# Performance work log

Measured on AMD Instinct MI355X. Metric: run time of the kernel, lower is better.

## Reference

```python
import jax, jax.numpy as jnp
import numpy as np

B, S, FEAT, HID, H = 8, 1024, 1024, 1024, 8
DH = HID // H  # head dim = 128
MASK_VAL = -128.0  # mask_val = -2**7 (soft additive mask, per original code)


def setup_inputs() -> dict:
    key = jax.random.key(0)
    ks = jax.random.split(key, 4)
    scale = 0.02
    return {
        "queries": jax.random.normal(ks[0], (B, S, FEAT), dtype=jnp.float32),
        "Wq": jax.random.normal(ks[1], (FEAT, HID), dtype=jnp.float32) * scale,
        "bq": jnp.zeros((HID,), dtype=jnp.float32),
        "Wk": jax.random.normal(ks[2], (FEAT, HID), dtype=jnp.float32) * scale,
        "bk": jnp.zeros((HID,), dtype=jnp.float32),
        "Wv": jax.random.normal(ks[3], (FEAT, HID), dtype=jnp.float32) * scale,
        "bv": jnp.zeros((HID,), dtype=jnp.float32),
    }


def reference(queries, Wq, bq, Wk, bk, Wv, bv):
    # Self-attention: keys = values = queries (torch forward defaults)
    q = queries @ Wq + bq  # [B,S,HID]
    k = queries @ Wk + bk
    v = queries @ Wv + bv
    # split heads: chunk along last dim == reshape (B,S,H,DH)
    qh = q.reshape(B, S, H, DH)
    kh = k.reshape(B, S, H, DH)
    vh = v.reshape(B, S, H, DH)
    # exp-scaled-dot score (non-standard: exp BEFORE mask/softmax)
    logits = jnp.einsum("bqhd,bkhd->bhqk", qh, kh) / np.float32(np.sqrt(DH))
    score = jnp.exp(logits)
    # soft additive causal mask: upper triangle (diag=1) gets -128
    mask = jnp.triu(jnp.full((S, S), MASK_VAL, dtype=score.dtype), k=1)
    att = jax.nn.softmax(score + mask, axis=-1)  # [B,H,S,S]
    ctx = jnp.einsum("bhqk,bkhd->bqhd", att, vh)  # [B,S,H,DH]
    # reverse heads: concat along last dim
    return ctx.reshape(B, S, HID)
```

## Files before the change

kernel.cpp:

```cpp
#include <hip/hip_runtime.h>


typedef __bf16 bf16x8 __attribute__((ext_vector_type(8)));
typedef float floatx4 __attribute__((ext_vector_type(4)));
typedef unsigned short u16;
typedef unsigned int u32;

#define RSCALE 0.08838834764831845f

__device__ __forceinline__ u16 f2b(float f) {
  union { float f; unsigned u; } v; v.f = f;
  return (u16)((v.u + 0x7FFFu + ((v.u >> 16) & 1u)) >> 16);
}

__device__ __forceinline__ void gld_lds16(const void* g, void* l) {
  __builtin_amdgcn_global_load_lds(
      (const __attribute__((address_space(1))) unsigned*)g,
      (__attribute__((address_space(3))) unsigned*)l, 16, 0, 0);
}

#define MFMA16(a, b, c) __builtin_amdgcn_mfma_f32_16x16x32_bf16(a, b, c, 0, 0, 0)

__global__ __launch_bounds__(256) void prep_kernel(
    const float4* __restrict__ X, u16* __restrict__ Xb,
    const float* __restrict__ Wq, const float* __restrict__ Wk,
    const float* __restrict__ Wv, u16* __restrict__ Wtb) {
  if (blockIdx.x < 8192) {
    unsigned i = blockIdx.x * 256u + threadIdx.x;
    float4 v = X[i];
    ushort4 o;
    o.x = f2b(v.x); o.y = f2b(v.y); o.z = f2b(v.z); o.w = f2b(v.w);
    *reinterpret_cast<ushort4*>(Xb + 4u * i) = o;
  } else {
    const int bid = blockIdx.x - 8192;
    const int mat = bid >> 10;
    const int bx = bid & 31, by = (bid >> 5) & 31;
    const float* W = (mat == 0) ? Wq : (mat == 1) ? Wk : Wv;
    u16* Wt = Wtb + (size_t)mat * (1024u * 1024u);
    __shared__ u16 tile[32][33];
    const int x = threadIdx.x & 31, y = threadIdx.x >> 5;
    const int kt = bx * 32, nt = by * 32;
#pragma unroll
    for (int i = 0; i < 4; ++i)
      tile[y + 8 * i][x] = f2b(W[(size_t)(kt + y + 8 * i) * 1024 + nt + x]);
    __syncthreads();
#pragma unroll
    for (int i = 0; i < 4; ++i)
      Wt[(size_t)(nt + y + 8 * i) * 1024 + kt + x] = tile[x][y + 8 * i];
  }
}

__global__ __launch_bounds__(256, 2) void gemm_qkv_kernel(
    const u16* __restrict__ Xb, const u16* __restrict__ Wtb,
    const float* __restrict__ bq, const float* __restrict__ bk,
    const float* __restrict__ bv, u16* __restrict__ Qh, u16* __restrict__ Kh,
    u16* __restrict__ Vt) {
  const int mat = blockIdx.z;
  const u16* __restrict__ Wt = Wtb + (size_t)mat * (1024u * 1024u);
  const float* __restrict__ bias = (mat == 0) ? bq : (mat == 1) ? bk : bv;

  const int m0 = blockIdx.x * 128;
  const int n0 = blockIdx.y * 128;

  __shared__ u16 As[2][128 * 64];
  __shared__ u16 Bs[2][128 * 64];

  const int tid = threadIdx.x;
  const int wid = tid >> 6;
  const int lane = tid & 63;
  const int quad = lane >> 4;
  const int l16 = lane & 15;
  const int wm = (wid & 1) * 64;
  const int wn = (wid >> 1) * 64;

  const floatx4 z4 = {0.f, 0.f, 0.f, 0.f};
  floatx4 acc[4][4];
#pragma unroll
  for (int i = 0; i < 4; ++i)
#pragma unroll
    for (int j = 0; j < 4; ++j) acc[i][j] = z4;

  const int srow = wid * 32;
  const int lrow = lane >> 3;
  const int gblk = (lane & 7) ^ lrow;

  auto stage = [&](int b, int k0) {
#pragma unroll
    for (int c = 0; c < 4; ++c) {
      const int row = srow + c * 8 + lrow;
      gld_lds16(Xb + (size_t)(m0 + row) * 1024 + k0 + gblk * 8,
                As[b] + (srow + c * 8) * 64);
      gld_lds16(Wt + (size_t)(n0 + row) * 1024 + k0 + gblk * 8,
                Bs[b] + (srow + c * 8) * 64);
    }
  };

  stage(0, 0);

  for (int i = 0; i < 16; ++i) {
    __syncthreads();
    if (i < 15) stage((i + 1) & 1, (i + 1) * 64);

    const u16* __restrict__ Ab = As[i & 1];
    const u16* __restrict__ Bb = Bs[i & 1];
#pragma unroll
    for (int c = 0; c < 2; ++c) {
      const int phys = ((c * 4 + quad) ^ (l16 & 7)) * 8;
      bf16x8 af[4], bfr[4];
#pragma unroll
      for (int ii = 0; ii < 4; ++ii)
        af[ii] = *(const bf16x8*)(Ab + (wm + ii * 16 + l16) * 64 + phys);
#pragma unroll
      for (int j = 0; j < 4; ++j)
        bfr[j] = *(const bf16x8*)(Bb + (wn + j * 16 + l16) * 64 + phys);
#pragma unroll
      for (int ii = 0; ii < 4; ++ii)
#pragma unroll
        for (int j = 0; j < 4; ++j)
          acc[ii][j] = MFMA16(af[ii], bfr[j], acc[ii][j]);
    }
  }

  const int b = m0 >> 10;
  const int h = n0 >> 7;
  const int sbase = (m0 & 1023) + wm;
  float bv4[4];
#pragma unroll
  for (int j = 0; j < 4; ++j) bv4[j] = bias[n0 + wn + j * 16 + l16];

  if (mat < 2) {
    u16* outp = (mat == 0 ? Qh : Kh) + (size_t)(b * 8 + h) * 1024 * 128;
#pragma unroll
    for (int i = 0; i < 4; ++i)
#pragma unroll
      for (int j = 0; j < 4; ++j) {
        const int d = wn + j * 16 + l16;
#pragma unroll
        for (int r = 0; r < 4; ++r) {
          const int s = sbase + i * 16 + quad * 4 + r;
          outp[(size_t)s * 128 + d] = f2b(acc[i][j][r] + bv4[j]);
        }
      }
  } else {
    u16* outp = Vt + (size_t)(b * 8 + h) * 128 * 1024;
#pragma unroll
    for (int i = 0; i < 4; ++i)
#pragma unroll
      for (int j = 0; j < 4; ++j) {
        const int d = wn + j * 16 + l16;
        const int s = sbase + i * 16 + quad * 4;
        ushort4 pk;
        pk.x = f2b(acc[i][j][0] + bv4[j]);
        pk.y = f2b(acc[i][j][1] + bv4[j]);
        pk.z = f2b(acc[i][j][2] + bv4[j]);
        pk.w = f2b(acc[i][j][3] + bv4[j]);
        *(ushort4*)(outp + (size_t)d * 1024 + s) = pk;
      }
  }
}

__global__ __launch_bounds__(256, 2) void attn_kernel(const u16* __restrict__ Qh,
                                                      const u16* __restrict__ Kh,
                                                      const u16* __restrict__ Vt,
                                                      float* __restrict__ out) {
  const int id = blockIdx.x;
  const int x = id & 7;
  const int j = id >> 3;
  const int bh = x * 8 + (j & 7);
  const int QTMAP[8] = {7, 5, 6, 4, 0, 2, 1, 3};
  const int qt = QTMAP[j >> 3];
  const int q0 = qt * 128;

  const int tid = threadIdx.x;
  const int wid = tid >> 6;
  const int lane = tid & 63;
  const int quad = lane >> 4;
  const int l16 = lane & 15;

  __shared__ u16 Ks[2][64 * 128];
  __shared__ u16 Vs[2][128 * 64];
  __shared__ u16 Ps[4][32 * 32];

  const u16* __restrict__ Qbase = Qh + (size_t)bh * 1024 * 128;
  const u16* __restrict__ Kbase = Kh + (size_t)bh * 1024 * 128;
  const u16* __restrict__ Vbase = Vt + (size_t)bh * 128 * 1024;

  const int qw = q0 + wid * 32;

  bf16x8 qf[2][4];
#pragma unroll
  for (int nt = 0; nt < 2; ++nt)
#pragma unroll
    for (int c = 0; c < 4; ++c)
      qf[nt][c] = *(const bf16x8*)(Qbase + (size_t)(qw + nt * 16 + l16) * 128 +
                                   c * 32 + quad * 8);

  const floatx4 z4 = {0.f, 0.f, 0.f, 0.f};
  floatx4 o[2][8];
#pragma unroll
  for (int nt = 0; nt < 2; ++nt)
#pragma unroll
    for (int dt = 0; dt < 8; ++dt) o[nt][dt] = z4;
  float lacc[2] = {0.f, 0.f};

  auto stage = [&](int b, int k0) {
#pragma unroll
    for (int c = 0; c < 4; ++c) {
      const int r0 = wid * 16 + c * 4;
      const int row = r0 + quad;
      gld_lds16(Kbase + (size_t)(k0 + row) * 128 + ((l16 ^ (c * 4 + quad)) * 8),
                Ks[b] + r0 * 128);
    }
#pragma unroll
    for (int c = 0; c < 4; ++c) {
      const int r0 = wid * 32 + c * 8;
      const int row = r0 + (lane >> 3);
      gld_lds16(Vbase + (size_t)row * 1024 + k0 +
                    (((lane & 7) ^ ((lane >> 3) & 7)) * 8),
                Vs[b] + r0 * 64);
    }
  };

  const int n = (q0 + 128) >> 6;
  stage(0, 0);

  for (int i = 0; i < n; ++i) {
    const int k0 = i << 6;
    __syncthreads();
    if (i + 1 < n) stage((i + 1) & 1, k0 + 64);

    const u16* __restrict__ Kb = Ks[i & 1];
    const u16* __restrict__ Vb = Vs[i & 1];

#pragma unroll
    for (int half = 0; half < 2; ++half) {
      if (k0 + half * 32 > qw + 31) break;

#pragma unroll
      for (int f2 = 0; f2 < 2; ++f2) {
        const int f = half * 2 + f2;
        bf16x8 kf[4];
#pragma unroll
        for (int c = 0; c < 4; ++c)
          kf[c] = *(const bf16x8*)(Kb + (f * 16 + l16) * 128 +
                                   (((c * 4 + quad) ^ l16) * 8));
        floatx4 st[2];
#pragma unroll
        for (int nt = 0; nt < 2; ++nt) {
          st[nt] = z4;
#pragma unroll
          for (int c = 0; c < 4; ++c) st[nt] = MFMA16(kf[c], qf[nt][c], st[nt]);
        }
        const int kb = k0 + f * 16 + quad * 4;
#pragma unroll
        for (int nt = 0; nt < 2; ++nt) {
          const int qrow = qw + nt * 16 + l16;
          float p[4];
#pragma unroll
          for (int r = 0; r < 4; ++r) {
            const float e = fminf(__expf(st[nt][r] * RSCALE), 85.f);
            p[r] = (kb + r > qrow) ? 0.f : __expf(e);
          }
          lacc[nt] += (p[0] + p[1]) + (p[2] + p[3]);
          uint2 pk;
          pk.x = (u32)f2b(p[0]) | ((u32)f2b(p[1]) << 16);
          pk.y = (u32)f2b(p[2]) | ((u32)f2b(p[3]) << 16);
          *(uint2*)((char*)Ps[wid] + (nt * 16 + l16) * 64 +
                    (((f2 * 2 + (quad >> 1)) ^ (l16 & 3)) * 16) +
                    (quad & 1) * 8) = pk;
        }
      }
      asm volatile("s_waitcnt lgkmcnt(0)" ::: "memory");

      bf16x8 pa[2];
#pragma unroll
      for (int nt = 0; nt < 2; ++nt)
        pa[nt] = *(const bf16x8*)((char*)Ps[wid] + (nt * 16 + l16) * 64 +
                                  ((quad ^ (l16 & 3)) * 16));
#pragma unroll
      for (int dt = 0; dt < 8; ++dt) {
        const bf16x8 vf = *(const bf16x8*)(
            Vb + (dt * 16 + l16) * 64 +
            (((half * 4 + quad) ^ (l16 & 7)) * 8));
        o[0][dt] = MFMA16(vf, pa[0], o[0][dt]);
        o[1][dt] = MFMA16(vf, pa[1], o[1][dt]);
      }
    }
  }

  float linv[2];
#pragma unroll
  for (int nt = 0; nt < 2; ++nt) {
    float s = lacc[nt];
    s += __shfl_xor(s, 16);
    s += __shfl_xor(s, 32);
    linv[nt] = 1.0f / s;
  }

  float* outp = out + (size_t)(bh >> 3) * 1024 * 1024 + (bh & 7) * 128;
#pragma unroll
  for (int nt = 0; nt < 2; ++nt) {
    const int qrow = qw + nt * 16 + l16;
#pragma unroll
    for (int dt = 0; dt < 8; ++dt) {
      float4 v;
      v.x = o[nt][dt][0] * linv[nt];
      v.y = o[nt][dt][1] * linv[nt];
      v.z = o[nt][dt][2] * linv[nt];
      v.w = o[nt][dt][3] * linv[nt];
      *(float4*)(outp + (size_t)qrow * 1024 + dt * 16 + quad * 4) = v;
    }
  }
}

extern "C" void kernel_launch(void* const* d_in, const int* in_sizes, int n_in,
                              void* d_out, int out_size, void* d_ws,
                              size_t ws_size, hipStream_t stream) {
  const float* X = (const float*)d_in[0];
  const float* Wq = (const float*)d_in[1];
  const float* bq = (const float*)d_in[2];
  const float* Wk = (const float*)d_in[3];
  const float* bk = (const float*)d_in[4];
  const float* Wv = (const float*)d_in[5];
  const float* bv = (const float*)d_in[6];
  float* out = (float*)d_out;

  char* ws = (char*)d_ws;
  u16* Xb  = (u16*)(ws);
  u16* Wtb = (u16*)(ws + (16u << 20));
  u16* Qh  = (u16*)(ws + (22u << 20));
  u16* Kh  = (u16*)(ws + (38u << 20));
  u16* Vt  = (u16*)(ws + (54u << 20));

  prep_kernel<<<8192 + 3072, 256, 0, stream>>>((const float4*)X, Xb, Wq, Wk,
                                               Wv, Wtb);
  dim3 gg(64, 8, 3);
  gemm_qkv_kernel<<<gg, 256, 0, stream>>>(Xb, Wtb, bq, bk, bv, Qh, Kh, Vt);
  attn_kernel<<<512, 256, 0, stream>>>(Qh, Kh, Vt, out);
}
```

Measured before the change: 198.7 us.

## Keep P in registers via permuted V layout, fold scale into Wq, shrink KV tiles

The attention kernel no longer round-trips the probability tile through shared memory. It packs P directly into MFMA operand registers and reads V in a key order that matches the accumulator layout, which removes the LDS write, the wait and the reload. The KV tile shrinks from 64 to 32 keys, and the causal mask is applied only on the diagonal tile. The softmax scale and log2e are folded into Wq and the bias so that exp2 can be used directly. The bf16 conversion switches from round-to-nearest-even to cheaper round-half-up with perm packing, which changes numerics slightly, and the smaller tiles add more iterations and barriers.

```diff
diff --git a/kernel.cpp b/kernel.cpp
--- a/kernel.cpp
+++ b/kernel.cpp
@@ -3,14 +3,22 @@
 
 typedef __bf16 bf16x8 __attribute__((ext_vector_type(8)));
 typedef float floatx4 __attribute__((ext_vector_type(4)));
+typedef unsigned int u32x4 __attribute__((ext_vector_type(4)));
+typedef unsigned long long u64;
+typedef u64 u64x2 __attribute__((ext_vector_type(2)));
 typedef unsigned short u16;
 typedef unsigned int u32;
 
-#define RSCALE 0.08838834764831845f
-
-__device__ __forceinline__ u16 f2b(float f) {
-  union { float f; unsigned u; } v; v.f = f;
-  return (u16)((v.u + 0x7FFFu + ((v.u >> 16) & 1u)) >> 16);
+#define LOG2E 1.4426950408889634f
+#define QSCALE 0.12751743f
+#define PSEL 0x07060302u
+
+__device__ __forceinline__ u32 pkbf16(float lo, float hi) {
+  return __builtin_amdgcn_perm(__float_as_uint(hi) + 0x8000u,
+                               __float_as_uint(lo) + 0x8000u, PSEL);
+}
+__device__ __forceinline__ u16 b16(float f) {
+  return (u16)((__float_as_uint(f) + 0x8000u) >> 16);
 }
 
 __device__ __forceinline__ void gld_lds16(const void* g, void* l) {
@@ -28,21 +36,23 @@
   if (blockIdx.x < 8192) {
     unsigned i = blockIdx.x * 256u + threadIdx.x;
     float4 v = X[i];
-    ushort4 o;
-    o.x = f2b(v.x); o.y = f2b(v.y); o.z = f2b(v.z); o.w = f2b(v.w);
-    *reinterpret_cast<ushort4*>(Xb + 4u * i) = o;
+    uint2 o;
+    o.x = pkbf16(v.x, v.y);
+    o.y = pkbf16(v.z, v.w);
+    *reinterpret_cast<uint2*>(Xb + 4u * i) = o;
   } else {
     const int bid = blockIdx.x - 8192;
     const int mat = bid >> 10;
     const int bx = bid & 31, by = (bid >> 5) & 31;
     const float* W = (mat == 0) ? Wq : (mat == 1) ? Wk : Wv;
+    const float ws = (mat == 0) ? QSCALE : 1.0f;
     u16* Wt = Wtb + (size_t)mat * (1024u * 1024u);
     __shared__ u16 tile[32][33];
     const int x = threadIdx.x & 31, y = threadIdx.x >> 5;
     const int kt = bx * 32, nt = by * 32;
 #pragma unroll
     for (int i = 0; i < 4; ++i)
-      tile[y + 8 * i][x] = f2b(W[(size_t)(kt + y + 8 * i) * 1024 + nt + x]);
+      tile[y + 8 * i][x] = b16(W[(size_t)(kt + y + 8 * i) * 1024 + nt + x] * ws);
     __syncthreads();
 #pragma unroll
     for (int i = 0; i < 4; ++i)
@@ -58,6 +68,7 @@
   const int mat = blockIdx.z;
   const u16* __restrict__ Wt = Wtb + (size_t)mat * (1024u * 1024u);
   const float* __restrict__ bias = (mat == 0) ? bq : (mat == 1) ? bk : bv;
+  const float bscale = (mat == 0) ? QSCALE : 1.0f;
 
   const int m0 = blockIdx.x * 128;
   const int n0 = blockIdx.y * 128;
@@ -126,7 +137,7 @@
   const int sbase = (m0 & 1023) + wm;
   float bv4[4];
 #pragma unroll
-  for (int j = 0; j < 4; ++j) bv4[j] = bias[n0 + wn + j * 16 + l16];
+  for (int j = 0; j < 4; ++j) bv4[j] = bias[n0 + wn + j * 16 + l16] * bscale;
 
   if (mat < 2) {
     u16* outp = (mat == 0 ? Qh : Kh) + (size_t)(b * 8 + h) * 1024 * 128;
@@ -138,7 +149,7 @@
 #pragma unroll
         for (int r = 0; r < 4; ++r) {
           const int s = sbase + i * 16 + quad * 4 + r;
-          outp[(size_t)s * 128 + d] = f2b(acc[i][j][r] + bv4[j]);
+          outp[(size_t)s * 128 + d] = b16(acc[i][j][r] + bv4[j]);
         }
       }
   } else {
@@ -149,12 +160,10 @@
       for (int j = 0; j < 4; ++j) {
         const int d = wn + j * 16 + l16;
         const int s = sbase + i * 16 + quad * 4;
-        ushort4 pk;
-        pk.x = f2b(acc[i][j][0] + bv4[j]);
-        pk.y = f2b(acc[i][j][1] + bv4[j]);
-        pk.z = f2b(acc[i][j][2] + bv4[j]);
-        pk.w = f2b(acc[i][j][3] + bv4[j]);
-        *(ushort4*)(outp + (size_t)d * 1024 + s) = pk;
+        uint2 pk;
+        pk.x = pkbf16(acc[i][j][0] + bv4[j], acc[i][j][1] + bv4[j]);
+        pk.y = pkbf16(acc[i][j][2] + bv4[j], acc[i][j][3] + bv4[j]);
+        *(uint2*)(outp + (size_t)d * 1024 + s) = pk;
       }
   }
 }
@@ -164,11 +173,9 @@
                                                       const u16* __restrict__ Vt,
                                                       float* __restrict__ out) {
   const int id = blockIdx.x;
-  const int x = id & 7;
-  const int j = id >> 3;
-  const int bh = x * 8 + (j & 7);
-  const int QTMAP[8] = {7, 5, 6, 4, 0, 2, 1, 3};
-  const int qt = QTMAP[j >> 3];
+  const int bh = (id & 7) * 8 + ((id >> 3) & 7);
+  const int QTMAP[8] = {7, 4, 6, 5, 0, 3, 1, 2};
+  const int qt = QTMAP[id >> 6];
   const int q0 = qt * 128;
 
   const int tid = threadIdx.x;
@@ -177,9 +184,8 @@
   const int quad = lane >> 4;
   const int l16 = lane & 15;
 
-  __shared__ u16 Ks[2][64 * 128];
-  __shared__ u16 Vs[2][128 * 64];
-  __shared__ u16 Ps[4][32 * 32];
+  __shared__ u16 Ks[2][32 * 128];
+  __shared__ u16 Vs[2][128 * 32];
 
   const u16* __restrict__ Qbase = Qh + (size_t)bh * 1024 * 128;
   const u16* __restrict__ Kbase = Kh + (size_t)bh * 1024 * 128;
@@ -205,40 +211,37 @@
 
   auto stage = [&](int b, int k0) {
 #pragma unroll
-    for (int c = 0; c < 4; ++c) {
-      const int r0 = wid * 16 + c * 4;
+    for (int c = 0; c < 2; ++c) {
+      const int r0 = wid * 8 + c * 4;
       const int row = r0 + quad;
-      gld_lds16(Kbase + (size_t)(k0 + row) * 128 + ((l16 ^ (c * 4 + quad)) * 8),
+      gld_lds16(Kbase + (size_t)(k0 + row) * 128 + ((l16 ^ (row & 15)) * 8),
                 Ks[b] + r0 * 128);
     }
 #pragma unroll
-    for (int c = 0; c < 4; ++c) {
-      const int r0 = wid * 32 + c * 8;
-      const int row = r0 + (lane >> 3);
-      gld_lds16(Vbase + (size_t)row * 1024 + k0 +
-                    (((lane & 7) ^ ((lane >> 3) & 7)) * 8),
-                Vs[b] + r0 * 64);
+    for (int c = 0; c < 2; ++c) {
+      const int r0 = wid * 32 + c * 16;
+      const int row = r0 + (lane >> 2);
+      gld_lds16(Vbase + (size_t)row * 1024 + k0 + (lane & 3) * 8,
+                Vs[b] + r0 * 32);
     }
   };
 
-  const int n = (q0 + 128) >> 6;
+  const int n = (q0 + 128) >> 5;
   stage(0, 0);
 
   for (int i = 0; i < n; ++i) {
-    const int k0 = i << 6;
+    const int k0 = i << 5;
     __syncthreads();
-    if (i + 1 < n) stage((i + 1) & 1, k0 + 64);
-
-    const u16* __restrict__ Kb = Ks[i & 1];
-    const u16* __restrict__ Vb = Vs[i & 1];
-
-#pragma unroll
-    for (int half = 0; half < 2; ++half) {
-      if (k0 + half * 32 > qw + 31) break;
-
-#pragma unroll
-      for (int f2 = 0; f2 < 2; ++f2) {
-        const int f = half * 2 + f2;
+    if (i + 1 < n) stage((i + 1) & 1, k0 + 32);
+
+    if (k0 <= qw + 31) {
+      const u16* __restrict__ Kb = Ks[i & 1];
+      const u16* __restrict__ Vb = Vs[i & 1];
+      const bool diag = (k0 == qw);
+
+      u32 pw[2][4];
+#pragma unroll
+      for (int f = 0; f < 2; ++f) {
         bf16x8 kf[4];
 #pragma unroll
         for (int c = 0; c < 4; ++c)
@@ -251,37 +254,39 @@
 #pragma unroll
           for (int c = 0; c < 4; ++c) st[nt] = MFMA16(kf[c], qf[nt][c], st[nt]);
         }
-        const int kb = k0 + f * 16 + quad * 4;
 #pragma unroll
         for (int nt = 0; nt < 2; ++nt) {
-          const int qrow = qw + nt * 16 + l16;
           float p[4];
 #pragma unroll
           for (int r = 0; r < 4; ++r) {
-            const float e = fminf(__expf(st[nt][r] * RSCALE), 85.f);
-            p[r] = (kb + r > qrow) ? 0.f : __expf(e);
+            const float e = fminf(__builtin_amdgcn_exp2f(st[nt][r]), 85.f);
+            p[r] = __builtin_amdgcn_exp2f(e * LOG2E);
+          }
+          if (diag) {
+#pragma unroll
+            for (int r = 0; r < 4; ++r)
+              p[r] = (f * 16 + quad * 4 + r > nt * 16 + l16) ? 0.f : p[r];
           }
           lacc[nt] += (p[0] + p[1]) + (p[2] + p[3]);
-          uint2 pk;
-          pk.x = (u32)f2b(p[0]) | ((u32)f2b(p[1]) << 16);
-          pk.y = (u32)f2b(p[2]) | ((u32)f2b(p[3]) << 16);
-          *(uint2*)((char*)Ps[wid] + (nt * 16 + l16) * 64 +
-                    (((f2 * 2 + (quad >> 1)) ^ (l16 & 3)) * 16) +
-                    (quad & 1) * 8) = pk;
+          pw[nt][f * 2 + 0] = pkbf16(p[0], p[1]);
+          pw[nt][f * 2 + 1] = pkbf16(p[2], p[3]);
         }
       }
-      asm volatile("s_waitcnt lgkmcnt(0)" ::: "memory");
 
       bf16x8 pa[2];
 #pragma unroll
-      for (int nt = 0; nt < 2; ++nt)
-        pa[nt] = *(const bf16x8*)((char*)Ps[wid] + (nt * 16 + l16) * 64 +
-                                  ((quad ^ (l16 & 3)) * 16));
+      for (int nt = 0; nt < 2; ++nt) {
+        u32x4 t;
+        t.x = pw[nt][0]; t.y = pw[nt][1]; t.z = pw[nt][2]; t.w = pw[nt][3];
+        pa[nt] = __builtin_bit_cast(bf16x8, t);
+      }
 #pragma unroll
       for (int dt = 0; dt < 8; ++dt) {
-        const bf16x8 vf = *(const bf16x8*)(
-            Vb + (dt * 16 + l16) * 64 +
-            (((half * 4 + quad) ^ (l16 & 7)) * 8));
+        const int d = dt * 16 + l16;
+        u64x2 t;
+        t.x = *(const u64*)(Vb + d * 32 + quad * 4);
+        t.y = *(const u64*)(Vb + d * 32 + 16 + quad * 4);
+        const bf16x8 vf = __builtin_bit_cast(bf16x8, t);
         o[0][dt] = MFMA16(vf, pa[0], o[0][dt]);
         o[1][dt] = MFMA16(vf, pa[1], o[1][dt]);
       }
```

Result: slower. 220.1 us (+10.8%).
